# Performance work log

Hardware: AMD Instinct MI355X
Metric: run time of the kernel (lower is better)

Reference implementation:

```python
import jax, jax.numpy as jnp
import numpy as np

N, E, G = 200000, 600000, 1024
NF_IN, EF_IN, H = 32, 16, 512
BN_EPS = 1e-5


def _bn(x, gamma, beta):
    # eval-mode BatchNorm1d with running_mean=0, running_var=1
    return x * (gamma / jnp.sqrt(1.0 + BN_EPS)) + beta


def setup_inputs() -> dict:
    key = jax.random.key(0)
    ks = jax.random.split(key, 32)
    s = 0.05
    inp = {
        'nf': jax.random.normal(ks[0], (N, NF_IN), jnp.float32),
        'ef': jax.random.normal(ks[1], (E, EF_IN), jnp.float32),
        'gf': jax.random.normal(ks[2], (G, H), jnp.float32),
        'device_params': jax.random.uniform(ks[3], (N,), jnp.float32),
        'node_y': jax.random.randint(ks[4], (N,), 0, 9),
        'batch_idx': jnp.sort(jax.random.randint(ks[5], (N,), 0, G)),
        'edge_index': jax.random.randint(ks[6], (2, E), 0, N),
        'nf_w1': jax.random.normal(ks[7], (NF_IN + 9, H), jnp.float32) * s,
        'nf_b1': jax.random.normal(ks[8], (H,), jnp.float32) * s,
        'nf_g1': jax.random.uniform(ks[9], (H,), jnp.float32, 0.5, 1.5),
        'nf_be1': jax.random.normal(ks[10], (H,), jnp.float32) * s,
        'nf_w2': jax.random.normal(ks[11], (H, H), jnp.float32) * s,
        'nf_b2': jax.random.normal(ks[12], (H,), jnp.float32) * s,
        'ef_w1': jax.random.normal(ks[13], (EF_IN, H), jnp.float32) * s,
        'ef_b1': jax.random.normal(ks[14], (H,), jnp.float32) * s,
        'ef_g1': jax.random.uniform(ks[15], (H,), jnp.float32, 0.5, 1.5),
        'ef_be1': jax.random.normal(ks[16], (H,), jnp.float32) * s,
        'ef_w2': jax.random.normal(ks[17], (H, H), jnp.float32) * s,
        'ef_b2': jax.random.normal(ks[18], (H,), jnp.float32) * s,
        'ow1': jax.random.normal(ks[19], (H, H), jnp.float32) * s,
        'ob1': jax.random.normal(ks[20], (H,), jnp.float32) * s,
        'og1': jax.random.uniform(ks[21], (H,), jnp.float32, 0.5, 1.5),
        'obe1': jax.random.normal(ks[22], (H,), jnp.float32) * s,
        'ow2': jax.random.normal(ks[23], (H, H), jnp.float32) * s,
        'ob2': jax.random.normal(ks[24], (H,), jnp.float32) * s,
        'og2': jax.random.uniform(ks[25], (H,), jnp.float32, 0.5, 1.5),
        'obe2': jax.random.normal(ks[26], (H,), jnp.float32) * s,
        'ow3': jax.random.normal(ks[27], (H, 2), jnp.float32) * s,
        'ob3': jax.random.normal(ks[28], (2,), jnp.float32) * s,
    }
    return inp


def reference(nf, ef, gf, device_params, node_y, batch_idx, edge_index,
              nf_w1, nf_b1, nf_g1, nf_be1, nf_w2, nf_b2,
              ef_w1, ef_b1, ef_g1, ef_be1, ef_w2, ef_b2,
              ow1, ob1, og1, obe1, ow2, ob2, og2, obe2, ow3, ob3):
    num_graphs = gf.shape[0]
    gelu = lambda x: jax.nn.gelu(x, approximate=False)  # torch nn.GELU default

    # DeviceParam_MLP: augment node features with scaled one-hot of node class
    nf_aug = jnp.concatenate(
        [nf, jax.nn.one_hot(node_y, 9, dtype=nf.dtype) * device_params[:, None]],
        axis=-1)  # [N, nf_in+9]
    h_n = gelu(_bn(nf_aug @ nf_w1 + nf_b1, nf_g1, nf_be1)) @ nf_w2 + nf_b2  # [N,H]
    h_e = gelu(_bn(ef @ ef_w1 + ef_b1, ef_g1, ef_be1)) @ ef_w2 + ef_b2      # [E,H]

    # two scatter_add pools into graph features
    gh = gf
    gh = gh + jax.ops.segment_sum(h_n, batch_idx, num_segments=num_graphs)
    edge_graph = batch_idx[edge_index[0]]  # graph id of each edge's source node
    gh = gh + jax.ops.segment_sum(h_e, edge_graph, num_segments=num_graphs)

    # output MLP (layer_num=3): two hidden blocks + final Linear -> 2
    x = gelu(_bn(gh @ ow1 + ob1, og1, obe1))
    x = gelu(_bn(x @ ow2 + ob2, og2, obe2))
    return x @ ow3 + ob3  # [G, 2]
```

## Files before the change

kernel.cpp:

```cpp
#include <hip/hip_runtime.h>
#include <hip/hip_bf16.h>

#define NN 200000
#define NE 600000
#define NG 1024
#define HH 512
#define ECAP 1024

typedef short short8 __attribute__((ext_vector_type(8)));
typedef float f32x4 __attribute__((ext_vector_type(4)));
typedef float f32x2 __attribute__((ext_vector_type(2)));
typedef float f32x16 __attribute__((ext_vector_type(16)));

__device__ __forceinline__ unsigned short f2bf(float f){
  unsigned u = __float_as_uint(f);
  u += 0x7fffu + ((u >> 16) & 1u);
  return (unsigned short)(u >> 16);
}
__device__ __forceinline__ float bf2f(unsigned short h){
  return __uint_as_float(((unsigned)h) << 16);
}

__device__ __forceinline__ short8 cvt8pk(float4 a, float4 b){
  union { short8 s; __hip_bfloat162 h[4]; } u;
  u.h[0] = __float22bfloat162_rn(make_float2(a.x, a.y));
  u.h[1] = __float22bfloat162_rn(make_float2(a.z, a.w));
  u.h[2] = __float22bfloat162_rn(make_float2(b.x, b.y));
  u.h[3] = __float22bfloat162_rn(make_float2(b.z, b.w));
  return u.s;
}

__device__ __forceinline__ void split8(const float* v, short8* hi, short8* lo){
  union { short8 s; __hip_bfloat162 h[4]; unsigned u[4]; } H, L;
#pragma unroll
  for (int p=0;p<4;++p){
    float a = v[2*p], b = v[2*p+1];
    H.h[p] = __float22bfloat162_rn(make_float2(a, b));
    unsigned hu = H.u[p];
    L.h[p] = __float22bfloat162_rn(make_float2(a - __uint_as_float(hu << 16),
                                               b - __uint_as_float(hu & 0xffff0000u)));
  }
  *hi = H.s; *lo = L.s;
}

__device__ __forceinline__ float gelu_f(float x){
  float p = __builtin_fmaf(x*x, -0.10294325f, -2.3022085f);
  float e = __builtin_amdgcn_exp2f(x * p);
  return x * __builtin_amdgcn_rcpf(1.0f + e);
}

__device__ __forceinline__ void g2(f32x2 xp, f32x2& aX, f32x2& aP,
    float C0, float C1, float C2, float C3, float C4, float C5, float C6, float C7){
  f32x2 s = __builtin_elementwise_fma(xp, xp, (f32x2)(-1.0f));
  f32x2 p = __builtin_elementwise_fma(s, (f32x2)C7, (f32x2)C6);
  p = __builtin_elementwise_fma(p, s, (f32x2)C5);
  p = __builtin_elementwise_fma(p, s, (f32x2)C4);
  p = __builtin_elementwise_fma(p, s, (f32x2)C3);
  p = __builtin_elementwise_fma(p, s, (f32x2)C2);
  p = __builtin_elementwise_fma(p, s, (f32x2)C1);
  p = __builtin_elementwise_fma(p, s, (f32x2)C0);
  aX += xp; aP += p;
}

#define ISQ 0.35355339059327376f
#define SQ2 1.41421356237309505f

__global__ __launch_bounds__(256) void kpre(
    const float* __restrict__ nfw1, const float* __restrict__ nfb1,
    const float* __restrict__ nfg1, const float* __restrict__ nfbe1,
    const float* __restrict__ efw1, const float* __restrict__ efb1,
    const float* __restrict__ efg1, const float* __restrict__ efbe1,
    unsigned short* __restrict__ w1n48T, unsigned short* __restrict__ w1eT16,
    float* __restrict__ b1n_s, float* __restrict__ b1e_s,
    const int* __restrict__ bidx, int* __restrict__ nstart,
    int* __restrict__ cnt, float* __restrict__ pcoef,
    const float* __restrict__ nf, const float* __restrict__ dp,
    const int* __restrict__ ny, const float* __restrict__ ef,
    unsigned short* __restrict__ nf48, unsigned short* __restrict__ efb){
  const float rs = 0.99999500003750f;
  int b = blockIdx.x, t = threadIdx.x;
  if (b < 2){
    int c = b*256 + t;
    float sc = efg1[c]*rs*ISQ;
#pragma unroll
    for (int k=0;k<16;++k) w1eT16[c*16+k] = f2bf(efw1[k*HH+c]*sc);
    b1e_s[c] = (efb1[c]*efg1[c]*rs + efbe1[c])*ISQ;
  } else if (b < 4){
    int c = (b-2)*256 + t;
    float sc = nfg1[c]*rs*ISQ;
#pragma unroll
    for (int k=0;k<48;++k)
      w1n48T[c*48+k] = (k < 41) ? f2bf(nfw1[k*HH+c]*sc) : (unsigned short)0;
    b1n_s[c] = (nfb1[c]*nfg1[c]*rs + nfbe1[c])*ISQ;
  } else if (b < 786){
    int i = (b-4)*256 + t;
    if (i < NN){
      int g0 = bidx[i];
      int g1 = (i+1 < NN) ? bidx[i+1] : NG;
      for (int g = g0+1; g <= g1; ++g) nstart[g] = i+1;
      if (i == 0) for (int g = 0; g <= g0; ++g) nstart[g] = 0;
    }
  } else if (b == 786){
    cnt[t] = 0; cnt[t+256] = 0; cnt[t+512] = 0; cnt[t+768] = 0;
    if (t == 0){
      double th[8], fj[8];
      for (int j=0;j<8;++j){
        th[j] = 3.14159265358979323846*((double)j + 0.5)/8.0;
        double cs = cos(th[j]);
        double u = 8.0*(cs + 1.0);
        double v = sqrt(u);
        fj[j] = 0.5*v*erf(v*0.70710678118654752);
      }
      double c[8];
      for (int k=0;k<8;++k){
        double sm = 0.0;
        for (int j=0;j<8;++j) sm += fj[j]*cos((double)k*th[j]);
        c[k] = 0.25*sm;
      }
      c[0] *= 0.5;
      const double T[8][8] = {
        { 1, 0,  0,  0,   0,    0,  0,  0},
        { 0, 1,  0,  0,   0,    0,  0,  0},
        {-1, 0,  2,  0,   0,    0,  0,  0},
        { 0,-3,  0,  4,   0,    0,  0,  0},
        { 1, 0, -8,  0,   8,    0,  0,  0},
        { 0, 5,  0,-20,   0,   16,  0,  0},
        {-1, 0, 18,  0, -48,    0, 32,  0},
        { 0,-7,  0, 56,   0, -112,  0, 64}};
      double m[8] = {0,0,0,0,0,0,0,0};
      for (int k=0;k<8;++k)
        for (int i=0;i<8;++i) m[i] += c[k]*T[k][i];
      double p0 = m[0]-m[1]+m[2]-m[3]+m[4]-m[5]+m[6]-m[7];
      m[0] -= p0;
      for (int i=0;i<8;++i) pcoef[i] = (float)m[i];
    }
  } else if (b < 1569){
    int r = (b-787)*256 + t;
    if (r < NN){
      const float4* ap = (const float4*)(nf + (size_t)r*32);
      unsigned short v[48];
      union { short8 s; unsigned short u[8]; } cv;
#pragma unroll
      for (int p2=0; p2<4; ++p2){
        cv.s = cvt8pk(ap[2*p2], ap[2*p2+1]);
#pragma unroll
        for (int j=0;j<8;++j) v[p2*8+j] = cv.u[j];
      }
      unsigned short db = f2bf(dp[r]);
      int cls = ny[r];
#pragma unroll
      for (int j=0;j<9;++j) v[32+j] = (cls==j) ? db : (unsigned short)0;
#pragma unroll
      for (int j=41;j<48;++j) v[j] = 0;
      unsigned short* op = nf48 + (size_t)r*48;
#pragma unroll
      for (int p2=0; p2<6; ++p2) *(short8*)(op + p2*8) = *(short8*)&v[p2*8];
    }
  } else {
    int r = (b-1569)*256 + t;
    if (r < NE){
      const float4* ap = (const float4*)(ef + (size_t)r*16);
      unsigned short* op = efb + (size_t)r*16;
      *(short8*)op       = cvt8pk(ap[0], ap[1]);
      *(short8*)(op + 8) = cvt8pk(ap[2], ap[3]);
    }
  }
}

__global__ __launch_bounds__(1024) void kscatter(const int* __restrict__ eidx,
    const int* __restrict__ bidx, int* __restrict__ eg,
    int* __restrict__ cnt, int* __restrict__ perm2d){
  __shared__ int h[NG];
  __shared__ int base[NG];
  const int b = blockIdx.x, t = threadIdx.x;
  h[t] = 0;
  __syncthreads();
  const int per = NE / 64;
  const int lo = b*per, hi = lo + per;
  for (int e = lo + t; e < hi; e += 1024){
    int g = bidx[eidx[e]];
    eg[e] = g;
    atomicAdd(&h[g], 1);
  }
  __syncthreads();
  int c = h[t];
  if (c > 0) base[t] = atomicAdd(&cnt[t], c);
  h[t] = 0;
  __syncthreads();
  for (int e = lo + t; e < hi; e += 1024){
    int g = eg[e];
    int p = base[g] + atomicAdd(&h[g], 1);
    if (p < ECAP) perm2d[(g << 10) + p] = e;
  }
}

__global__ __launch_bounds__(512) void kedge(
    const unsigned short* __restrict__ efb, const int* __restrict__ perm2d,
    const int* __restrict__ cnt, const unsigned short* __restrict__ w1eT16,
    const float* __restrict__ b1e_s, const float* __restrict__ pcoef,
    float* __restrict__ S){
  __shared__ short lds[2][32*40];
  const int t = threadIdx.x;
  const int lane = t & 63, wid = t >> 6;
  const int hi = lane >> 5;
  const int g = blockIdx.x >> 1;
  const int col = ((blockIdx.x & 1) << 8) + (wid << 5) + (lane & 31);
  const float C0 = pcoef[0], C1 = pcoef[1], C2 = pcoef[2], C3 = pcoef[3];
  const float C4 = pcoef[4], C5 = pcoef[5], C6 = pcoef[6], C7 = pcoef[7];
  short8 bfr = *(const short8*)(w1eT16 + col*16 + (hi<<3));
  float bv = b1e_s[col];
  f32x16 bias16;
#pragma unroll
  for (int i=0;i<16;++i) bias16[i] = bv;
  f32x2 aX = {0.f,0.f}, aP = {0.f,0.f};
  const int s1 = cnt[g];
  if (s1 > 0){
    const int base = g << 10;
    const int nch = (s1 + 31) >> 5;
    short8 a1;
    if (t < 64){
      int r0 = min(t & 31, s1-1);
      int r1 = min(32 + (t & 31), s1-1);
      int e0 = perm2d[base + r0];
      int e1 = perm2d[base + r1];
      short8 a0 = *(const short8*)(efb + (size_t)e0*16 + ((t>>5)<<3));
      *(short8*)&lds[0][(t&31)*40 + ((t>>5)<<3)] = a0;
      a1 = *(const short8*)(efb + (size_t)e1*16 + ((t>>5)<<3));
    }
    __syncthreads();
    for (int ch=0; ch<nch; ++ch){
      short8 af = *(const short8*)&lds[ch&1][(lane&31)*40 + (hi<<3)];
      if (t < 64){
        if (ch+1 < nch) *(short8*)&lds[(ch+1)&1][(t&31)*40 + ((t>>5)<<3)] = a1;
        int r2 = min((ch+2)*32 + (t & 31), s1-1);
        int e2 = perm2d[base + r2];
        a1 = *(const short8*)(efb + (size_t)e2*16 + ((t>>5)<<3));
      }
      __syncthreads();
      f32x16 acc = __builtin_amdgcn_mfma_f32_32x32x16_bf16(af, bfr, bias16, 0, 0, 0);
      const int vr = s1 - ch*32;
      if (vr >= 32){
#pragma unroll
        for (int i=0;i<8;++i){
          f32x2 xp = {acc[2*i], acc[2*i+1]};
          g2(xp, aX, aP, C0,C1,C2,C3,C4,C5,C6,C7);
        }
      } else {
#pragma unroll
        for (int i=0;i<8;++i){
          int r0 = ((2*i)&3) + (((2*i)>>2)<<3) + (hi<<2);
          f32x2 xp = { (r0 < vr) ? acc[2*i] : 0.f,
                       (r0+1 < vr) ? acc[2*i+1] : 0.f };
          g2(xp, aX, aP, C0,C1,C2,C3,C4,C5,C6,C7);
        }
      }
    }
  }
  float ssum = __builtin_fmaf(SQ2, aX[0]+aX[1], aP[0]+aP[1]);
  ssum += __shfl_xor(ssum, 32);
  if (lane < 32) S[(size_t)g*1024 + 512 + col] = ssum;
}

__global__ __launch_bounds__(256) void knode(
    const unsigned short* __restrict__ nf48, const int* __restrict__ nstart,
    const unsigned short* __restrict__ w1n48T, const float* __restrict__ b1n_s,
    const float* __restrict__ pcoef, float* __restrict__ S){
  const int t = threadIdx.x;
  const int lane = t & 63, wid = t >> 6;
  const int hi = lane >> 5;
  const int g = blockIdx.x >> 2;
  const int col = ((blockIdx.x & 3) << 7) + (wid << 5) + (lane & 31);
  const float C0 = pcoef[0], C1 = pcoef[1], C2 = pcoef[2], C3 = pcoef[3];
  const float C4 = pcoef[4], C5 = pcoef[5], C6 = pcoef[6], C7 = pcoef[7];
  const unsigned short* bp = w1n48T + col*48 + (hi<<3);
  short8 bf0 = *(const short8*)(bp);
  short8 bf1 = *(const short8*)(bp + 16);
  short8 bf2 = *(const short8*)(bp + 32);
  float bv = b1n_s[col];
  f32x16 bias16;
#pragma unroll
  for (int i=0;i<16;++i) bias16[i] = bv;
  f32x2 aX = {0.f,0.f}, aP = {0.f,0.f};
  const int s0 = nstart[g], s1 = nstart[g+1];
  const int nch = (s1 - s0 + 31) >> 5;
  for (int ch=0; ch<nch; ++ch){
    int rb = s0 + ch*32;
    int ar = min(rb + (lane & 31), s1-1);
    const unsigned short* apn = nf48 + (size_t)ar*48 + (hi<<3);
    short8 a0 = *(const short8*)(apn);
    short8 a1 = *(const short8*)(apn + 16);
    short8 a2 = *(const short8*)(apn + 32);
    f32x16 acc = __builtin_amdgcn_mfma_f32_32x32x16_bf16(a0, bf0, bias16, 0, 0, 0);
    acc = __builtin_amdgcn_mfma_f32_32x32x16_bf16(a1, bf1, acc, 0, 0, 0);
    acc = __builtin_amdgcn_mfma_f32_32x32x16_bf16(a2, bf2, acc, 0, 0, 0);
    const int vr = s1 - rb;
    if (vr >= 32){
#pragma unroll
      for (int i=0;i<8;++i){
        f32x2 xp = {acc[2*i], acc[2*i+1]};
        g2(xp, aX, aP, C0,C1,C2,C3,C4,C5,C6,C7);
      }
    } else {
#pragma unroll
      for (int i=0;i<8;++i){
        int r0 = ((2*i)&3) + (((2*i)>>2)<<3) + (hi<<2);
        f32x2 xp = { (r0 < vr) ? acc[2*i] : 0.f,
                     (r0+1 < vr) ? acc[2*i+1] : 0.f };
        g2(xp, aX, aP, C0,C1,C2,C3,C4,C5,C6,C7);
      }
    }
  }
  float ssum = __builtin_fmaf(SQ2, aX[0]+aX[1], aP[0]+aP[1]);
  ssum += __shfl_xor(ssum, 32);
  if (lane < 32) S[(size_t)g*1024 + col] = ssum;
}

__global__ __launch_bounds__(256) void kgemm3(const float* __restrict__ A, int lda, int nkc,
    const float* __restrict__ B0, const float* __restrict__ B1,
    float* __restrict__ out,
    const float* __restrict__ gf, const int* __restrict__ nstart, const int* __restrict__ cnt,
    const float* __restrict__ b2n, const float* __restrict__ b2e,
    const float* __restrict__ bias, const float* __restrict__ gam, const float* __restrict__ bet){
  const int t = threadIdx.x, lane = t & 63, w = t >> 6;
  const int q = lane >> 4, m = lane & 15;
  const int c0 = blockIdx.x*16, r0 = blockIdx.y*64 + w*16;
  f32x4 acc = {0.f,0.f,0.f,0.f};
  const float* ap = A + (size_t)(r0 + m)*lda + (q<<3);
  for (int kc = 0; kc < nkc; ++kc){
    const int ko = kc*32;
    float4 x = *(const float4*)(ap + ko);
    float4 y = *(const float4*)(ap + ko + 4);
    float v[8] = {x.x,x.y,x.z,x.w,y.x,y.y,y.z,y.w};
    short8 ah, al;
    split8(v, &ah, &al);
    const float* Bp = (kc < 16) ? B0 : B1;
    const float* bp = Bp + (size_t)((kc & 15)*32 + (q<<3))*HH + c0 + m;
    float bvv[8];
#pragma unroll
    for (int j=0;j<8;++j) bvv[j] = bp[(size_t)j*HH];
    short8 bh, bl;
    split8(bvv, &bh, &bl);
    acc = __builtin_amdgcn_mfma_f32_16x16x32_bf16(ah, bh, acc, 0, 0, 0);
    acc = __builtin_amdgcn_mfma_f32_16x16x32_bf16(ah, bl, acc, 0, 0, 0);
    acc = __builtin_amdgcn_mfma_f32_16x16x32_bf16(al, bh, acc, 0, 0, 0);
  }
  const float rs = 0.99999500003750f;
  const int c = c0 + m;
  if (gf){
    const float bnv = b2n[c], bev = b2e[c];
#pragma unroll
    for (int i=0;i<4;++i){
      int r = r0 + q*4 + i;
      float cn = (float)(nstart[r+1] - nstart[r]);
      float ce = (float)cnt[r];
      out[(size_t)r*HH + c] = acc[i] + gf[(size_t)r*HH + c] + cn*bnv + ce*bev;
    }
  } else {
    const float sc = gam[c]*rs, bi = bias[c], be = bet[c];
#pragma unroll
    for (int i=0;i<4;++i){
      int r = r0 + q*4 + i;
      out[(size_t)r*HH + c] = gelu_f((acc[i] + bi)*sc + be);
    }
  }
}

__global__ __launch_bounds__(256) void kfinal(const float* __restrict__ x2, const float* __restrict__ w3,
    const float* __restrict__ b3, float* __restrict__ out){
  const int lane = threadIdx.x & 63, wv = threadIdx.x >> 6;
  const int r = blockIdx.x*4 + wv;
  float a0 = 0.f, a1 = 0.f;
#pragma unroll
  for (int tt=0; tt<8; ++tt){
    int k = lane + tt*64;
    float x = x2[(size_t)r*HH + k];
    a0 = __builtin_fmaf(x, w3[2*k], a0);
    a1 = __builtin_fmaf(x, w3[2*k+1], a1);
  }
#pragma unroll
  for (int d=1; d<64; d<<=1){ a0 += __shfl_xor(a0, d); a1 += __shfl_xor(a1, d); }
  if (lane == 0){ out[r*2] = a0 + b3[0]; out[r*2+1] = a1 + b3[1]; }
}

extern "C" void kernel_launch(void* const* d_in, const int* in_sizes, int n_in,
                              void* d_out, int out_size, void* d_ws, size_t ws_size,
                              hipStream_t stream) {
  const float* nf    = (const float*)d_in[0];
  const float* ef    = (const float*)d_in[1];
  const float* gf    = (const float*)d_in[2];
  const float* dp    = (const float*)d_in[3];
  const int*   ny    = (const int*)d_in[4];
  const int*   bidx  = (const int*)d_in[5];
  const int*   eidx  = (const int*)d_in[6];
  const float* nfw1  = (const float*)d_in[7];
  const float* nfb1  = (const float*)d_in[8];
  const float* nfg1  = (const float*)d_in[9];
  const float* nfbe1 = (const float*)d_in[10];
  const float* w2n   = (const float*)d_in[11];
  const float* b2n   = (const float*)d_in[12];
  const float* efw1  = (const float*)d_in[13];
  const float* efb1  = (const float*)d_in[14];
  const float* efg1  = (const float*)d_in[15];
  const float* efbe1 = (const float*)d_in[16];
  const float* w2e   = (const float*)d_in[17];
  const float* b2e   = (const float*)d_in[18];
  const float* ow1   = (const float*)d_in[19];
  const float* ob1   = (const float*)d_in[20];
  const float* og1   = (const float*)d_in[21];
  const float* obe1  = (const float*)d_in[22];
  const float* ow2   = (const float*)d_in[23];
  const float* ob2   = (const float*)d_in[24];
  const float* og2   = (const float*)d_in[25];
  const float* obe2  = (const float*)d_in[26];
  const float* ow3   = (const float*)d_in[27];
  const float* ob3   = (const float*)d_in[28];

  unsigned char* p = (unsigned char*)d_ws;
  float* S      = (float*)p;                 p += (size_t)NG*1024*4;
  int*   perm2d = (int*)p;                   p += (size_t)NG*ECAP*4;
  unsigned short* nf48 = (unsigned short*)p; p += (size_t)NN*48*2;
  unsigned short* efb  = (unsigned short*)p; p += (size_t)NE*16*2;
  unsigned short* w1n48T = (unsigned short*)p; p += 512*48*2;
  unsigned short* w1eT16 = (unsigned short*)p; p += 512*16*2;
  float* b1n_s  = (float*)p;                 p += 512*4;
  float* b1e_s  = (float*)p;                 p += 512*4;
  int* nstart   = (int*)p;                   p += 1032*4;
  int* cnt      = (int*)p;                   p += NG*4;
  float* pcoef  = (float*)p;                 p += 64;
  int* eg = (int*)S;
  float* gh  = (float*)nf48;
  float* xg2 = gh  + (size_t)NG*HH;
  float* x2f = xg2 + (size_t)NG*HH;

  kpre<<<3913, 256, 0, stream>>>(nfw1, nfb1, nfg1, nfbe1, efw1, efb1, efg1, efbe1,
                                 w1n48T, w1eT16, b1n_s, b1e_s, bidx, nstart, cnt,
                                 pcoef, nf, dp, ny, ef, nf48, efb);
  kscatter<<<64, 1024, 0, stream>>>(eidx, bidx, eg, cnt, perm2d);
  kedge<<<2048, 512, 0, stream>>>(efb, perm2d, cnt, w1eT16, b1e_s, pcoef, S);
  knode<<<4096, 256, 0, stream>>>(nf48, nstart, w1n48T, b1n_s, pcoef, S);
  kgemm3<<<dim3(32,16), 256, 0, stream>>>(S, 1024, 32, w2n, w2e, gh,
                                          gf, nstart, cnt, b2n, b2e,
                                          nullptr, nullptr, nullptr);
  kgemm3<<<dim3(32,16), 256, 0, stream>>>(gh, 512, 16, ow1, ow1, xg2,
                                          nullptr, nullptr, nullptr, nullptr, nullptr,
                                          ob1, og1, obe1);
  kgemm3<<<dim3(32,16), 256, 0, stream>>>(xg2, 512, 16, ow2, ow2, x2f,
                                          nullptr, nullptr, nullptr, nullptr, nullptr,
                                          ob2, og2, obe2);
  kfinal<<<NG/4, 256, 0, stream>>>(x2f, ow3, ob3, (float*)d_out);
}
```

Before: 341.1 us.

## Fuse edge and node pooling kernels, pre-split GEMM weights, use packed FMA GELU

Merges the edge and node first-layer pooling kernels into one launch. The edge path loses its LDS double buffering and now gathers rows directly, and node blocks switch to 512 threads handling 256 columns. The kpre kernel gains extra blocks that transpose the second-layer and output MLP weights once and split them into bf16 hi/lo arrays, so kgemm3 reads short8 vectors instead of doing strided fp32 loads and converting in the inner loop. The GELU polynomial is rewritten with inline v_pk_fma_f32 asm. This trades extra workspace and preprocessing work for less redundant weight conversion and one fewer launch.

```diff
diff --git a/kernel.cpp b/kernel.cpp
--- a/kernel.cpp
+++ b/kernel.cpp
@@ -8,6 +8,7 @@
 #define ECAP 1024
 
 typedef short short8 __attribute__((ext_vector_type(8)));
+typedef short short4v __attribute__((ext_vector_type(4)));
 typedef float f32x4 __attribute__((ext_vector_type(4)));
 typedef float f32x2 __attribute__((ext_vector_type(2)));
 typedef float f32x16 __attribute__((ext_vector_type(16)));
@@ -49,18 +50,24 @@
   return x * __builtin_amdgcn_rcpf(1.0f + e);
 }
 
-__device__ __forceinline__ void g2(f32x2 xp, f32x2& aX, f32x2& aP,
-    float C0, float C1, float C2, float C3, float C4, float C5, float C6, float C7){
-  f32x2 s = __builtin_elementwise_fma(xp, xp, (f32x2)(-1.0f));
-  f32x2 p = __builtin_elementwise_fma(s, (f32x2)C7, (f32x2)C6);
-  p = __builtin_elementwise_fma(p, s, (f32x2)C5);
-  p = __builtin_elementwise_fma(p, s, (f32x2)C4);
-  p = __builtin_elementwise_fma(p, s, (f32x2)C3);
-  p = __builtin_elementwise_fma(p, s, (f32x2)C2);
-  p = __builtin_elementwise_fma(p, s, (f32x2)C1);
-  p = __builtin_elementwise_fma(p, s, (f32x2)C0);
-  aX += xp; aP += p;
-}
+#define PKFMA3(d,a,b,c) asm("v_pk_fma_f32 %0, %1, %2, %3" : "=v"(d) : "v"(a), "v"(b), "v"(c))
+#define PKFMA_IP(p,s,k) asm("v_pk_fma_f32 %0, %0, %1, %2" : "+v"(p) : "v"(s), "v"(k))
+#define PKADD_IP(d,a)   asm("v_pk_add_f32 %0, %0, %1"     : "+v"(d) : "v"(a))
+
+#define G2(y_) { \
+  f32x2 s_; PKFMA3(s_, y_, y_, n1); \
+  f32x2 p_; PKFMA3(p_, s_, K7, K6); \
+  PKFMA_IP(p_, s_, K5); PKFMA_IP(p_, s_, K4); \
+  PKFMA_IP(p_, s_, K3); PKFMA_IP(p_, s_, K2); \
+  PKFMA_IP(p_, s_, K1); PKFMA_IP(p_, s_, K0); \
+  PKADD_IP(aX, y_); PKADD_IP(aP, p_); }
+
+#define COEFS \
+  const float C0 = pcoef[0], C1 = pcoef[1], C2 = pcoef[2], C3 = pcoef[3]; \
+  const float C4 = pcoef[4], C5 = pcoef[5], C6 = pcoef[6], C7 = pcoef[7]; \
+  const f32x2 K0 = {C0,C0}, K1 = {C1,C1}, K2 = {C2,C2}, K3 = {C3,C3}; \
+  const f32x2 K4 = {C4,C4}, K5 = {C5,C5}, K6 = {C6,C6}, K7 = {C7,C7}; \
+  const f32x2 n1 = {-1.f,-1.f};
 
 #define ISQ 0.35355339059327376f
 #define SQ2 1.41421356237309505f
@@ -70,13 +77,18 @@
     const float* __restrict__ nfg1, const float* __restrict__ nfbe1,
     const float* __restrict__ efw1, const float* __restrict__ efb1,
     const float* __restrict__ efg1, const float* __restrict__ efbe1,
+    const float* __restrict__ w2n, const float* __restrict__ w2e,
+    const float* __restrict__ ow1, const float* __restrict__ ow2,
     unsigned short* __restrict__ w1n48T, unsigned short* __restrict__ w1eT16,
     float* __restrict__ b1n_s, float* __restrict__ b1e_s,
     const int* __restrict__ bidx, int* __restrict__ nstart,
     int* __restrict__ cnt, float* __restrict__ pcoef,
     const float* __restrict__ nf, const float* __restrict__ dp,
     const int* __restrict__ ny, const float* __restrict__ ef,
-    unsigned short* __restrict__ nf48, unsigned short* __restrict__ efb){
+    unsigned short* __restrict__ nf48, unsigned short* __restrict__ efb,
+    unsigned short* __restrict__ Bh1, unsigned short* __restrict__ Bl1,
+    unsigned short* __restrict__ Bh2, unsigned short* __restrict__ Bl2,
+    unsigned short* __restrict__ Bh3, unsigned short* __restrict__ Bl3){
   const float rs = 0.99999500003750f;
   int b = blockIdx.x, t = threadIdx.x;
   if (b < 2){
@@ -156,13 +168,51 @@
 #pragma unroll
       for (int p2=0; p2<6; ++p2) *(short8*)(op + p2*8) = *(short8*)&v[p2*8];
     }
-  } else {
+  } else if (b < 3913){
     int r = (b-1569)*256 + t;
     if (r < NE){
       const float4* ap = (const float4*)(ef + (size_t)r*16);
       unsigned short* op = efb + (size_t)r*16;
       *(short8*)op       = cvt8pk(ap[0], ap[1]);
       *(short8*)(op + 8) = cvt8pk(ap[2], ap[3]);
+    }
+  } else {
+    __shared__ float lds[64][65];
+    int tb = b - 3913;
+    int which, KK; unsigned short *Th, *Tl;
+    if (tb < 128){ which = 1; KK = 1024; Th = Bh1; Tl = Bl1; }
+    else if (tb < 192){ which = 2; KK = 512; Th = Bh2; Tl = Bl2; tb -= 128; }
+    else { which = 3; KK = 512; Th = Bh3; Tl = Bl3; tb -= 192; }
+    const int kt = tb >> 3, ct = tb & 7;
+    const int k0 = kt*64, c0 = ct*64;
+    const int tr = t >> 4, tc = (t & 15)*4;
+#pragma unroll
+    for (int i=0;i<4;++i){
+      int row = tr + i*16;
+      int gk = k0 + row;
+      const float* src;
+      if (which == 1) src = (gk < 512) ? (w2n + (size_t)gk*HH) : (w2e + (size_t)(gk-512)*HH);
+      else if (which == 2) src = ow1 + (size_t)gk*HH;
+      else src = ow2 + (size_t)gk*HH;
+      float4 v = *(const float4*)(src + c0 + tc);
+      lds[row][tc+0] = v.x; lds[row][tc+1] = v.y;
+      lds[row][tc+2] = v.z; lds[row][tc+3] = v.w;
+    }
+    __syncthreads();
+#pragma unroll
+    for (int i=0;i<4;++i){
+      int c = tr + i*16;
+      short4v h4, l4;
+#pragma unroll
+      for (int j=0;j<4;++j){
+        float vv = lds[tc+j][c];
+        unsigned short h = f2bf(vv);
+        h4[j] = (short)h;
+        l4[j] = (short)f2bf(vv - bf2f(h));
+      }
+      size_t o = (size_t)(c0 + c)*KK + k0 + tc;
+      *(short4v*)(Th + o) = h4;
+      *(short4v*)(Tl + o) = l4;
     }
   }
 }
@@ -194,129 +244,105 @@
   }
 }
 
-__global__ __launch_bounds__(512) void kedge(
+__global__ __launch_bounds__(512) void kmain2(
     const unsigned short* __restrict__ efb, const int* __restrict__ perm2d,
     const int* __restrict__ cnt, const unsigned short* __restrict__ w1eT16,
-    const float* __restrict__ b1e_s, const float* __restrict__ pcoef,
-    float* __restrict__ S){
-  __shared__ short lds[2][32*40];
-  const int t = threadIdx.x;
-  const int lane = t & 63, wid = t >> 6;
-  const int hi = lane >> 5;
-  const int g = blockIdx.x >> 1;
-  const int col = ((blockIdx.x & 1) << 8) + (wid << 5) + (lane & 31);
-  const float C0 = pcoef[0], C1 = pcoef[1], C2 = pcoef[2], C3 = pcoef[3];
-  const float C4 = pcoef[4], C5 = pcoef[5], C6 = pcoef[6], C7 = pcoef[7];
-  short8 bfr = *(const short8*)(w1eT16 + col*16 + (hi<<3));
-  float bv = b1e_s[col];
-  f32x16 bias16;
-#pragma unroll
-  for (int i=0;i<16;++i) bias16[i] = bv;
-  f32x2 aX = {0.f,0.f}, aP = {0.f,0.f};
-  const int s1 = cnt[g];
-  if (s1 > 0){
-    const int base = g << 10;
-    const int nch = (s1 + 31) >> 5;
-    short8 a1;
-    if (t < 64){
-      int r0 = min(t & 31, s1-1);
-      int r1 = min(32 + (t & 31), s1-1);
-      int e0 = perm2d[base + r0];
-      int e1 = perm2d[base + r1];
-      short8 a0 = *(const short8*)(efb + (size_t)e0*16 + ((t>>5)<<3));
-      *(short8*)&lds[0][(t&31)*40 + ((t>>5)<<3)] = a0;
-      a1 = *(const short8*)(efb + (size_t)e1*16 + ((t>>5)<<3));
-    }
-    __syncthreads();
-    for (int ch=0; ch<nch; ++ch){
-      short8 af = *(const short8*)&lds[ch&1][(lane&31)*40 + (hi<<3)];
-      if (t < 64){
-        if (ch+1 < nch) *(short8*)&lds[(ch+1)&1][(t&31)*40 + ((t>>5)<<3)] = a1;
-        int r2 = min((ch+2)*32 + (t & 31), s1-1);
-        int e2 = perm2d[base + r2];
-        a1 = *(const short8*)(efb + (size_t)e2*16 + ((t>>5)<<3));
-      }
-      __syncthreads();
-      f32x16 acc = __builtin_amdgcn_mfma_f32_32x32x16_bf16(af, bfr, bias16, 0, 0, 0);
-      const int vr = s1 - ch*32;
-      if (vr >= 32){
-#pragma unroll
-        for (int i=0;i<8;++i){
-          f32x2 xp = {acc[2*i], acc[2*i+1]};
-          g2(xp, aX, aP, C0,C1,C2,C3,C4,C5,C6,C7);
-        }
-      } else {
-#pragma unroll
-        for (int i=0;i<8;++i){
-          int r0 = ((2*i)&3) + (((2*i)>>2)<<3) + (hi<<2);
-          f32x2 xp = { (r0 < vr) ? acc[2*i] : 0.f,
-                       (r0+1 < vr) ? acc[2*i+1] : 0.f };
-          g2(xp, aX, aP, C0,C1,C2,C3,C4,C5,C6,C7);
-        }
-      }
-    }
-  }
-  float ssum = __builtin_fmaf(SQ2, aX[0]+aX[1], aP[0]+aP[1]);
-  ssum += __shfl_xor(ssum, 32);
-  if (lane < 32) S[(size_t)g*1024 + 512 + col] = ssum;
-}
-
-__global__ __launch_bounds__(256) void knode(
+    const float* __restrict__ b1e_s,
     const unsigned short* __restrict__ nf48, const int* __restrict__ nstart,
     const unsigned short* __restrict__ w1n48T, const float* __restrict__ b1n_s,
     const float* __restrict__ pcoef, float* __restrict__ S){
   const int t = threadIdx.x;
   const int lane = t & 63, wid = t >> 6;
-  const int hi = lane >> 5;
-  const int g = blockIdx.x >> 2;
-  const int col = ((blockIdx.x & 3) << 7) + (wid << 5) + (lane & 31);
-  const float C0 = pcoef[0], C1 = pcoef[1], C2 = pcoef[2], C3 = pcoef[3];
-  const float C4 = pcoef[4], C5 = pcoef[5], C6 = pcoef[6], C7 = pcoef[7];
-  const unsigned short* bp = w1n48T + col*48 + (hi<<3);
-  short8 bf0 = *(const short8*)(bp);
-  short8 bf1 = *(const short8*)(bp + 16);
-  short8 bf2 = *(const short8*)(bp + 32);
-  float bv = b1n_s[col];
-  f32x16 bias16;
-#pragma unroll
-  for (int i=0;i<16;++i) bias16[i] = bv;
+  const int hi = lane >> 5, ln31 = lane & 31;
+  COEFS;
   f32x2 aX = {0.f,0.f}, aP = {0.f,0.f};
-  const int s0 = nstart[g], s1 = nstart[g+1];
-  const int nch = (s1 - s0 + 31) >> 5;
-  for (int ch=0; ch<nch; ++ch){
-    int rb = s0 + ch*32;
-    int ar = min(rb + (lane & 31), s1-1);
-    const unsigned short* apn = nf48 + (size_t)ar*48 + (hi<<3);
-    short8 a0 = *(const short8*)(apn);
-    short8 a1 = *(const short8*)(apn + 16);
-    short8 a2 = *(const short8*)(apn + 32);
-    f32x16 acc = __builtin_amdgcn_mfma_f32_32x32x16_bf16(a0, bf0, bias16, 0, 0, 0);
-    acc = __builtin_amdgcn_mfma_f32_32x32x16_bf16(a1, bf1, acc, 0, 0, 0);
-    acc = __builtin_amdgcn_mfma_f32_32x32x16_bf16(a2, bf2, acc, 0, 0, 0);
-    const int vr = s1 - rb;
-    if (vr >= 32){
+  if (blockIdx.x < 2048){
+    const int g = blockIdx.x >> 1;
+    const int col = ((blockIdx.x & 1) << 8) + (wid << 5) + ln31;
+    short8 bfr = *(const short8*)(w1eT16 + col*16 + (hi<<3));
+    const float bv = b1e_s[col];
+    f32x16 bias16;
+#pragma unroll
+    for (int i=0;i<16;++i) bias16[i] = bv;
+    const int s1 = min(cnt[g], ECAP);
+    const int base = g << 10;
+    const int nfull = s1 >> 5;
+    int rb = 0;
+    for (int ch=0; ch<nfull; ++ch, rb += 32){
+      int e = perm2d[base + rb + ln31];
+      short8 af = *(const short8*)(efb + (size_t)e*16 + (hi<<3));
+      f32x16 acc = __builtin_amdgcn_mfma_f32_32x32x16_bf16(af, bfr, bias16, 0, 0, 0);
 #pragma unroll
       for (int i=0;i<8;++i){
-        f32x2 xp = {acc[2*i], acc[2*i+1]};
-        g2(xp, aX, aP, C0,C1,C2,C3,C4,C5,C6,C7);
-      }
-    } else {
+        f32x2 y = {acc[2*i], acc[2*i+1]};
+        G2(y);
+      }
+    }
+    if (rb < s1){
+      int e = perm2d[base + min(rb + ln31, s1-1)];
+      short8 af = *(const short8*)(efb + (size_t)e*16 + (hi<<3));
+      f32x16 acc = __builtin_amdgcn_mfma_f32_32x32x16_bf16(af, bfr, bias16, 0, 0, 0);
+      const int vr = s1 - rb;
 #pragma unroll
       for (int i=0;i<8;++i){
         int r0 = ((2*i)&3) + (((2*i)>>2)<<3) + (hi<<2);
-        f32x2 xp = { (r0 < vr) ? acc[2*i] : 0.f,
-                     (r0+1 < vr) ? acc[2*i+1] : 0.f };
-        g2(xp, aX, aP, C0,C1,C2,C3,C4,C5,C6,C7);
-      }
-    }
-  }
-  float ssum = __builtin_fmaf(SQ2, aX[0]+aX[1], aP[0]+aP[1]);
-  ssum += __shfl_xor(ssum, 32);
-  if (lane < 32) S[(size_t)g*1024 + col] = ssum;
+        f32x2 y = { (r0 < vr) ? acc[2*i] : 0.f,
+                    (r0+1 < vr) ? acc[2*i+1] : 0.f };
+        G2(y);
+      }
+    }
+    float ssum = __builtin_fmaf(SQ2, aX[0]+aX[1], aP[0]+aP[1]);
+    ssum += __shfl_xor(ssum, 32);
+    if (lane < 32) S[(size_t)g*1024 + 512 + col] = ssum;
+  } else {
+    const int b2 = blockIdx.x - 2048;
+    const int g = b2 >> 1;
+    const int col = ((b2 & 1) << 8) + (wid << 5) + ln31;
+    const unsigned short* bp = w1n48T + col*48 + (hi<<3);
+    short8 b0 = *(const short8*)(bp);
+    short8 b1 = *(const short8*)(bp + 16);
+    short8 b2f = *(const short8*)(bp + 32);
+    const float bv = b1n_s[col];
+    f32x16 bias16;
+#pragma unroll
+    for (int i=0;i<16;++i) bias16[i] = bv;
+    const int s0r = nstart[g], s1 = nstart[g+1];
+    const int nch = (s1 - s0r + 31) >> 5;
+    for (int ch=0; ch<nch; ++ch){
+      const int rb = s0r + ch*32;
+      int ar = min(rb + ln31, s1-1);
+      const unsigned short* apn = nf48 + (size_t)ar*48 + (hi<<3);
+      short8 a0 = *(const short8*)(apn);
+      short8 a1 = *(const short8*)(apn + 16);
+      short8 a2 = *(const short8*)(apn + 32);
+      f32x16 acc = __builtin_amdgcn_mfma_f32_32x32x16_bf16(a0, b0, bias16, 0, 0, 0);
+      acc = __builtin_amdgcn_mfma_f32_32x32x16_bf16(a1, b1, acc, 0, 0, 0);
+      acc = __builtin_amdgcn_mfma_f32_32x32x16_bf16(a2, b2f, acc, 0, 0, 0);
+      const int vr = s1 - rb;
+      if (vr >= 32){
+#pragma unroll
+        for (int i=0;i<8;++i){
+          f32x2 y = {acc[2*i], acc[2*i+1]};
+          G2(y);
+        }
+      } else {
+#pragma unroll
+        for (int i=0;i<8;++i){
+          int r0 = ((2*i)&3) + (((2*i)>>2)<<3) + (hi<<2);
+          f32x2 y = { (r0 < vr) ? acc[2*i] : 0.f,
+                      (r0+1 < vr) ? acc[2*i+1] : 0.f };
+          G2(y);
+        }
+      }
+    }
+    float ssum = __builtin_fmaf(SQ2, aX[0]+aX[1], aP[0]+aP[1]);
+    ssum += __shfl_xor(ssum, 32);
+    if (lane < 32) S[(size_t)g*1024 + col] = ssum;
+  }
 }
 
 __global__ __launch_bounds__(256) void kgemm3(const float* __restrict__ A, int lda, int nkc,
-    const float* __restrict__ B0, const float* __restrict__ B1,
+    const unsigned short* __restrict__ BhT, const unsigned short* __restrict__ BlT,
     float* __restrict__ out,
     const float* __restrict__ gf, const int* __restrict__ nstart, const int* __restrict__ cnt,
     const float* __restrict__ b2n, const float* __restrict__ b2e,
@@ -324,8 +350,11 @@
   const int t = threadIdx.x, lane = t & 63, w = t >> 6;
   const int q = lane >> 4, m = lane & 15;
   const int c0 = blockIdx.x*16, r0 = blockIdx.y*64 + w*16;
+  const int K = nkc*32;
   f32x4 acc = {0.f,0.f,0.f,0.f};
   const float* ap = A + (size_t)(r0 + m)*lda + (q<<3);
+  const unsigned short* bhp = BhT + (size_t)(c0 + m)*K + (q<<3);
+  const unsigned short* blp = BlT + (size_t)(c0 + m)*K + (q<<3);
   for (int kc = 0; kc < nkc; ++kc){
     const int ko = kc*32;
     float4 x = *(const float4*)(ap + ko);
@@ -333,13 +362,8 @@
     float v[8] = {x.x,x.y,x.z,x.w,y.x,y.y,y.z,y.w};
     short8 ah, al;
     split8(v, &ah, &al);
-    const float* Bp = (kc < 16) ? B0 : B1;
-    const float* bp = Bp + (size_t)((kc & 15)*32 + (q<<3))*HH + c0 + m;
-    float bvv[8];
-#pragma unroll
-    for (int j=0;j<8;++j) bvv[j] = bp[(size_t)j*HH];
-    short8 bh, bl;
-    split8(bvv, &bh, &bl);
+    short8 bh = *(const short8*)(bhp + ko);
+    short8 bl = *(const short8*)(blp + ko);
     acc = __builtin_amdgcn_mfma_f32_16x16x32_bf16(ah, bh, acc, 0, 0, 0);
     acc = __builtin_amdgcn_mfma_f32_16x16x32_bf16(ah, bl, acc, 0, 0, 0);
     acc = __builtin_amdgcn_mfma_f32_16x16x32_bf16(al, bh, acc, 0, 0, 0);
@@ -420,6 +444,12 @@
   int*   perm2d = (int*)p;                   p += (size_t)NG*ECAP*4;
   unsigned short* nf48 = (unsigned short*)p; p += (size_t)NN*48*2;
   unsigned short* efb  = (unsigned short*)p; p += (size_t)NE*16*2;
+  unsigned short* Bh1 = (unsigned short*)p;  p += (size_t)HH*1024*2;
+  unsigned short* Bl1 = (unsigned short*)p;  p += (size_t)HH*1024*2;
+  unsigned short* Bh2 = (unsigned short*)p;  p += (size_t)HH*512*2;
+  unsigned short* Bl2 = (unsigned short*)p;  p += (size_t)HH*512*2;
+  unsigned short* Bh3 = (unsigned short*)p;  p += (size_t)HH*512*2;
+  unsigned short* Bl3 = (unsigned short*)p;  p += (size_t)HH*512*2;
   unsigned short* w1n48T = (unsigned short*)p; p += 512*48*2;
   unsigned short* w1eT16 = (unsigned short*)p; p += 512*16*2;
   float* b1n_s  = (float*)p;                 p += 512*4;
@@ -432,19 +462,21 @@
   float* xg2 = gh  + (size_t)NG*HH;
   float* x2f = xg2 + (size_t)NG*HH;
 
-  kpre<<<3913, 256, 0, stream>>>(nfw1, nfb1, nfg1, nfbe1, efw1, efb1, efg1, efbe1,
+  kpre<<<4169, 256, 0, stream>>>(nfw1, nfb1, nfg1, nfbe1, efw1, efb1, efg1, efbe1,
+                                 w2n, w2e, ow1, ow2,
                                  w1n48T, w1eT16, b1n_s, b1e_s, bidx, nstart, cnt,
-                                 pcoef, nf, dp, ny, ef, nf48, efb);
+                                 pcoef, nf, dp, ny, ef, nf48, efb,
+                                 Bh1, Bl1, Bh2, Bl2, Bh3, Bl3);
   kscatter<<<64, 1024, 0, stream>>>(eidx, bidx, eg, cnt, perm2d);
-  kedge<<<2048, 512, 0, stream>>>(efb, perm2d, cnt, w1eT16, b1e_s, pcoef, S);
-  knode<<<4096, 256, 0, stream>>>(nf48, nstart, w1n48T, b1n_s, pcoef, S);
-  kgemm3<<<dim3(32,16), 256, 0, stream>>>(S, 1024, 32, w2n, w2e, gh,
+  kmain2<<<4096, 512, 0, stream>>>(efb, perm2d, cnt, w1eT16, b1e_s,
+                                   nf48, nstart, w1n48T, b1n_s, pcoef, S);
+  kgemm3<<<dim3(32,16), 256, 0, stream>>>(S, 1024, 32, Bh1, Bl1, gh,
                                           gf, nstart, cnt, b2n, b2e,
                                           nullptr, nullptr, nullptr);
-  kgemm3<<<dim3(32,16), 256, 0, stream>>>(gh, 512, 16, ow1, ow1, xg2,
+  kgemm3<<<dim3(32,16), 256, 0, stream>>>(gh, 512, 16, Bh2, Bl2, xg2,
                                           nullptr, nullptr, nullptr, nullptr, nullptr,
                                           ob1, og1, obe1);
-  kgemm3<<<dim3(32,16), 256, 0, stream>>>(xg2, 512, 16, ow2, ow2, x2f,
+  kgemm3<<<dim3(32,16), 256, 0, stream>>>(xg2, 512, 16, Bh3, Bl3, x2f,
                                           nullptr, nullptr, nullptr, nullptr, nullptr,
                                           ob2, og2, obe2);
   kfinal<<<NG/4, 256, 0, stream>>>(x2f, ow3, ob3, (float*)d_out);
```

Measured after the change: 358.5 us. 1.05x slower.
